# Kernel optimization log

Measured on AMD Instinct MI355X. Metric: run time of the kernel, lower is better.

## Reference

```python
import jax, jax.numpy as jnp
import numpy as np

B, N = 2, 2048
D_MODEL, HEADS = 512, 8
D_K = D_MODEL // HEADS
D_HIDDEN = 2048
MIN_SPREAD = 2.0
MIN_RBF = 1e-3
MAX_RBF = 1.0
LN_EPS = 1e-5


def setup_inputs() -> dict:
    key = jax.random.key(0)
    ks = jax.random.split(key, 12)
    xs = (6.0 / (D_K + D_MODEL)) ** 0.5
    q = jax.random.normal(ks[0], (B, N, D_MODEL), dtype=jnp.float32)
    k = jax.random.normal(ks[1], (B, N, D_MODEL), dtype=jnp.float32)
    v = jax.random.normal(ks[2], (B, N, D_MODEL), dtype=jnp.float32)
    coords = jax.random.normal(ks[3], (B, N, 3), dtype=jnp.float32) * 10.0
    mask = jnp.ones((B, N), dtype=bool)
    q_proj = jax.random.uniform(ks[4], (HEADS, D_MODEL, D_K), minval=-xs, maxval=xs)
    k_proj = jax.random.uniform(ks[5], (HEADS, D_MODEL, D_K), minval=-xs, maxval=xs)
    v_proj = jax.random.uniform(ks[6], (HEADS, D_MODEL, D_K), minval=-xs, maxval=xs)
    q_bias = jnp.zeros((HEADS, D_K))
    k_bias = jnp.zeros((HEADS, D_K))
    v_bias = jnp.zeros((HEADS, D_K))
    ow = (1.0 / D_MODEL) ** 0.5
    out_w = jax.random.uniform(ks[7], (D_MODEL, D_MODEL), minval=-ow, maxval=ow)
    spread_w = jnp.zeros((HEADS,))
    beta_w = jnp.zeros((HEADS,))
    ln1_g = jnp.ones((D_MODEL,)); ln1_b = jnp.zeros((D_MODEL,))
    ln2_g = jnp.ones((D_MODEL,)); ln2_b = jnp.zeros((D_MODEL,))
    w1 = jax.random.normal(ks[8], (D_MODEL, D_HIDDEN)) * 0.02
    b1 = jnp.zeros((D_HIDDEN,))
    w2 = jax.random.normal(ks[9], (D_HIDDEN, D_MODEL)) * 0.02
    b2 = jnp.zeros((D_MODEL,))
    return dict(q=q, k=k, v=v, coords=coords, mask=mask,
                q_proj=q_proj, k_proj=k_proj, v_proj=v_proj,
                q_bias=q_bias, k_bias=k_bias, v_bias=v_bias,
                out_w=out_w, spread_w=spread_w, beta_w=beta_w,
                ln1_g=ln1_g, ln1_b=ln1_b, ln2_g=ln2_g, ln2_b=ln2_b,
                w1=w1, b1=b1, w2=w2, b2=b2)


def _layernorm(x, g, b):
    mu = jnp.mean(x, axis=-1, keepdims=True)
    var = jnp.mean((x - mu) ** 2, axis=-1, keepdims=True)
    return (x - mu) * jax.lax.rsqrt(var + LN_EPS) * g + b


def _geo_attention(q, k, v, coords, mask,
                   q_proj, k_proj, v_proj, q_bias, k_bias, v_bias,
                   out_w, spread_w, beta_w):
    # per-head projections: [B,H,N,dk]
    Q = jnp.einsum('bnd,hdk->bhnk', q, q_proj) + q_bias[None, :, None, :]
    K = jnp.einsum('bnd,hdk->bhnk', k, k_proj) + k_bias[None, :, None, :]
    V = jnp.einsum('bnd,hdk->bhnk', v, v_proj) + v_bias[None, :, None, :]

    spreads = MIN_SPREAD + jnp.exp(spread_w)   # [H]
    betas = jnp.exp(beta_w)                    # [H]

    # pairwise squared distances [B,N,N]
    d2 = jnp.sum((coords[:, :, None, :] - coords[:, None, :, :]) ** 2, axis=-1)
    # per-head Gaussian RBF [B,H,N,N]
    rbf = jnp.exp(-d2[:, None, :, :] / (2.0 * spreads[None, :, None, None] ** 2))

    scores = jnp.einsum('bhnk,bhmk->bhnm', Q, K) / jnp.sqrt(jnp.float32(D_K))
    scores = betas[None, :, None, None] * rbf * scores

    # sparsity: keys with rbf outside [min_rbf, max_rbf] or padded are masked out
    valid = (rbf >= MIN_RBF) & (rbf <= MAX_RBF) & mask[:, None, None, :]
    scores = jnp.where(valid, scores, -jnp.inf)
    attn = jax.nn.softmax(scores, axis=-1)     # diagonal always valid (rbf=1)

    out = jnp.einsum('bhnm,bhmk->bhnk', attn, V)         # [B,H,N,dk]
    # torch: out.permute(0,2,3,1).reshape(B,N,d_model) -> (b,n,dk,h) layout
    out = jnp.transpose(out, (0, 2, 3, 1)).reshape(out.shape[0], out.shape[2], D_MODEL)
    return out @ out_w.T


def reference(q, k, v, coords, mask,
              q_proj, k_proj, v_proj, q_bias, k_bias, v_bias,
              out_w, spread_w, beta_w,
              ln1_g, ln1_b, ln2_g, ln2_b, w1, b1, w2, b2):
    attn_out = _geo_attention(q, k, v, coords, mask,
                              q_proj, k_proj, v_proj, q_bias, k_bias, v_bias,
                              out_w, spread_w, beta_w)
    x = _layernorm(q + attn_out, ln1_g, ln1_b)
    ffn = jax.nn.relu(x @ w1 + b1) @ w2 + b2
    x = _layernorm(x + ffn, ln2_g, ln2_b)
    return x
```

## Files before the change

### kernel.cpp

```cpp
#include <hip/hip_runtime.h>
#include <math.h>

typedef __attribute__((ext_vector_type(8))) short bf16x8;
typedef __attribute__((ext_vector_type(4))) float f32x4;

#define MFMA16(a,b,c) __builtin_amdgcn_mfma_f32_16x16x32_bf16((a),(b),(c),0,0,0)
#define LOG2E 1.44269504f

__device__ __forceinline__ unsigned short f2bf(float f) {
    union { float f; unsigned u; } x; x.f = f;
    unsigned r = x.u + 0x7FFFu + ((x.u >> 16) & 1u);
    return (unsigned short)(r >> 16);
}

__device__ __forceinline__ unsigned cvt_pk_bf16(float lo, float hi) {
    unsigned r;
    asm("v_cvt_pk_bf16_f32 %0, %1, %2" : "=v"(r) : "v"(lo), "v"(hi));
    return r;
}

__device__ __forceinline__ float exp2_fast(float x) {
    float r; asm("v_exp_f32 %0, %1" : "=v"(r) : "v"(x)); return r;
}

__device__ __forceinline__ void gload16(const unsigned short* g, unsigned short* l) {
    __builtin_amdgcn_global_load_lds(
        (const __attribute__((address_space(1))) void*)(unsigned long long)g,
        (__attribute__((address_space(3))) void*)(unsigned int)(unsigned long long)l,
        16, 0, 0);
}

__global__ __launch_bounds__(256) void cvt_qkv(
    const float* __restrict__ q, const float* __restrict__ k,
    const float* __restrict__ v,
    unsigned short* __restrict__ qb, unsigned short* __restrict__ kb,
    unsigned short* __restrict__ vb, int n)
{
    for (int i = blockIdx.x * 256 + threadIdx.x; i < n; i += gridDim.x * 256) {
        qb[i] = f2bf(q[i]); kb[i] = f2bf(k[i]); vb[i] = f2bf(v[i]);
    }
}

__global__ __launch_bounds__(256) void cvt_weights(
    const float* __restrict__ qp, const float* __restrict__ kp,
    const float* __restrict__ vp, const float* __restrict__ ow,
    const float* __restrict__ w1, const float* __restrict__ w2,
    const float* __restrict__ qbias, const float* __restrict__ kbias,
    const float* __restrict__ vbias,
    unsigned short* __restrict__ qpT, unsigned short* __restrict__ kpT,
    unsigned short* __restrict__ vpT, unsigned short* __restrict__ owT,
    unsigned short* __restrict__ w1T, unsigned short* __restrict__ w2T,
    float* __restrict__ biasC)
{
    const int NP = 262144;
    const int total = 4 * NP + 1048576 + 1048576 + 1536;
    for (int i = blockIdx.x * 256 + threadIdx.x; i < total; i += gridDim.x * 256) {
        if (i < 3 * NP) {
            int which = i / NP, r = i - which * NP;
            int n = r >> 9, d = r & 511;
            int h = n >> 6, kk = n & 63;
            const float* src = (which == 0) ? qp : (which == 1) ? kp : vp;
            unsigned short* dst = (which == 0) ? qpT : (which == 1) ? kpT : vpT;
            dst[r] = f2bf(src[(h << 15) + (d << 6) + kk]);
        } else if (i < 4 * NP) {
            int r = i - 3 * NP;
            int oi = r >> 9, f = r & 511;
            int h = f >> 6, kk = f & 63;
            owT[r] = f2bf(ow[(oi << 9) + (kk << 3) + h]);
        } else if (i < 4 * NP + 1048576) {
            int r = i - 4 * NP;
            int n = r >> 9, d = r & 511;
            w1T[r] = f2bf(w1[(d << 11) + n]);
        } else if (i < 4 * NP + 2097152) {
            int r = i - 4 * NP - 1048576;
            int n = r >> 11, d = r & 2047;
            w2T[r] = f2bf(w2[(d << 9) + n]);
        } else {
            int j = i - 4 * NP - 2097152;
            biasC[j] = (j < 512) ? qbias[j] : (j < 1024) ? kbias[j - 512] : vbias[j - 1024];
        }
    }
}

template<int BNT, int RELU, int SF32, int SB16, int SVTR, int SQKV>
__global__ __launch_bounds__(256) void gemm_bt(
    const unsigned short* __restrict__ Aq,
    const unsigned short* __restrict__ Ak,
    const unsigned short* __restrict__ Av,
    const unsigned short* __restrict__ Bt,
    const float* __restrict__ bias,
    float* __restrict__ Cf, unsigned short* __restrict__ Cb,
    unsigned short* __restrict__ Cb2, unsigned short* __restrict__ Cb3,
    int M, int N, int K)
{
    constexpr int BC = BNT / 32;
    __shared__ __align__(16) unsigned short As[128][64];
    __shared__ __align__(16) unsigned short Bs[BNT][64];
    const int tid = threadIdx.x;
    const int m0 = blockIdx.y << 7, n0 = blockIdx.x * BNT;
    const int wv = tid >> 6, lane = tid & 63;
    const int lrow = lane & 15, kg = lane >> 4;
    const int wr = (wv >> 1) << 6, wc = (wv & 1) * (BNT / 2);
    const int gr = lane >> 3, gc = (lane & 7) << 3;

    const unsigned short* A = Aq;
    if (SQKV) A = (n0 < 512) ? Aq : (n0 < 1024) ? Ak : Av;

    f32x4 acc[4][BC];
    const f32x4 z4 = {0.f, 0.f, 0.f, 0.f};
#pragma unroll
    for (int i = 0; i < 4; ++i)
#pragma unroll
        for (int j = 0; j < BC; ++j) acc[i][j] = z4;

    const int nkt = K >> 6;
    for (int kt = 0; kt < nkt; ++kt) {
        __syncthreads();
        const int k0 = kt << 6;
#pragma unroll
        for (int i = 0; i < 4; ++i) {
            const int r = (wv << 5) + (i << 3);
            gload16(&A[(long)(m0 + r + gr) * K + k0 + gc], &As[r][0]);
        }
#pragma unroll
        for (int i = 0; i < BNT / 32; ++i) {
            const int r = wv * (BNT / 4) + (i << 3);
            gload16(&Bt[(long)(n0 + r + gr) * K + k0 + gc], &Bs[r][0]);
        }
        __syncthreads();
#pragma unroll
        for (int ks = 0; ks < 2; ++ks) {
            const int koff = (ks << 5) + (kg << 3);
            bf16x8 af[4], bfr[BC];
#pragma unroll
            for (int mi = 0; mi < 4; ++mi)
                af[mi] = *(const bf16x8*)(&As[wr + (mi << 4) + lrow][koff]);
#pragma unroll
            for (int ni = 0; ni < BC; ++ni)
                bfr[ni] = *(const bf16x8*)(&Bs[wc + (ni << 4) + lrow][koff]);
#pragma unroll
            for (int mi = 0; mi < 4; ++mi)
#pragma unroll
                for (int ni = 0; ni < BC; ++ni)
                    acc[mi][ni] = MFMA16(af[mi], bfr[ni], acc[mi][ni]);
        }
    }

#pragma unroll
    for (int mi = 0; mi < 4; ++mi) {
#pragma unroll
        for (int ni = 0; ni < BC; ++ni) {
            const int col = n0 + wc + (ni << 4) + lrow;
            const float bv = bias ? bias[col] : 0.0f;
#pragma unroll
            for (int j = 0; j < 4; ++j) {
                const int row = m0 + wr + (mi << 4) + (kg << 2) + j;
                float val = acc[mi][ni][j] + bv;
                if (RELU) val = fmaxf(val, 0.0f);
                if (SF32) Cf[(long)row * N + col] = val;
                if (SB16) Cb[(long)row * N + col] = f2bf(val);
                if (SVTR)
                    Cb[((long)(row >> 11) << 20) + ((long)col << 11) + (row & 2047)] = f2bf(val);
                if (SQKV) {
                    if (n0 < 512)
                        Cb[(long)row * 512 + col] = f2bf(val);
                    else if (n0 < 1024)
                        Cb2[(long)row * 512 + (col - 512)] = f2bf(val);
                    else {
                        const int c2 = col - 1024;
                        Cb3[((long)(row >> 11) << 20) + ((long)c2 << 11) + (row & 2047)] = f2bf(val);
                    }
                }
            }
        }
    }
}

__global__ __launch_bounds__(256) void geo_attn(
    const unsigned short* __restrict__ Qh,
    const unsigned short* __restrict__ Kh,
    const unsigned short* __restrict__ VhT,
    const float* __restrict__ coords,
    const float* __restrict__ spread_w, const float* __restrict__ beta_w,
    unsigned short* __restrict__ Ob)
{
    __shared__ unsigned short Qs[64][72];
    __shared__ unsigned short Ks[64][72];
    __shared__ unsigned short Vs[64][72];
    __shared__ unsigned short Ps[4][16][72];
    __shared__ float4 ck4[64];

    const int tid = threadIdx.x;
    const int bid = blockIdx.x;
    const int swz = ((bid & 7) << 6) + (bid >> 3);
    const int bh = swz >> 5, qt = swz & 31;
    const int b = bh >> 3, h = bh & 7;
    const int wv = tid >> 6, lane = tid & 63;
    const int lq = lane & 15, kg = lane >> 4;
    const float NEG_INF = -__builtin_inff();
    const float THRL = 8.0f * LOG2E;
    const float RCUT = -9.96578428f;

    const float spread = 2.0f + __expf(spread_w[h]);
    const float inv2s2l = LOG2E / (2.0f * spread * spread);
    const float coefL = __expf(beta_w[h]) * 0.125f * LOG2E;

    {
        const long qbase = ((long)(b * 2048 + qt * 64)) * 512 + h * 64;
#pragma unroll
        for (int i = 0; i < 2; ++i) {
            int slot = tid + (i << 8);
            int r = slot >> 3, c = (slot & 7) << 3;
            *(int4*)(&Qs[r][c]) = *(const int4*)(&Qh[qbase + (long)r * 512 + c]);
        }
    }

    float cqx, cqy, cqz;
    {
        long ca = ((long)(b * 2048 + qt * 64 + wv * 16 + lq)) * 3;
        cqx = coords[ca]; cqy = coords[ca + 1]; cqz = coords[ca + 2];
    }

    float mrun = NEG_INF, lrun = 0.0f;
    f32x4 Oa[4];
    const f32x4 z4 = {0.f, 0.f, 0.f, 0.f};
#pragma unroll
    for (int nd = 0; nd < 4; ++nd) Oa[nd] = z4;

    const long kbase0 = ((long)b * 2048) * 512 + h * 64;
    const long vbase = ((long)(b * 8 + h)) * 131072;

    for (int kt = 0; kt < 32; ++kt) {
        __syncthreads();
        const int k0 = kt << 6;
#pragma unroll
        for (int i = 0; i < 2; ++i) {
            int slot = tid + (i << 8);
            int r = slot >> 3, c = (slot & 7) << 3;
            *(int4*)(&Ks[r][c]) = *(const int4*)(&Kh[kbase0 + (long)(k0 + r) * 512 + c]);
            *(int4*)(&Vs[r][c]) = *(const int4*)(&VhT[vbase + (long)r * 2048 + k0 + c]);
        }
        if (tid < 64) {
            long ca = ((long)(b * 2048 + k0 + tid)) * 3;
            ck4[tid] = make_float4(coords[ca], coords[ca + 1], coords[ca + 2], 0.0f);
        }
        __syncthreads();

        f32x4 t4[4];
#pragma unroll
        for (int ra = 0; ra < 4; ++ra) t4[ra] = z4;
#pragma unroll
        for (int ks = 0; ks < 2; ++ks) {
            const int koff = (ks << 5) + (kg << 3);
            bf16x8 bq = *(const bf16x8*)(&Qs[(wv << 4) + lq][koff]);
#pragma unroll
            for (int ra = 0; ra < 4; ++ra) {
                bf16x8 ak = *(const bf16x8*)(&Ks[(ra << 4) + lq][koff]);
                t4[ra] = MFMA16(ak, bq, t4[ra]);
            }
        }

        float tmax = NEG_INF;
#pragma unroll
        for (int ra = 0; ra < 4; ++ra) {
#pragma unroll
            for (int j = 0; j < 4; ++j) {
                float4 ck = ck4[(ra << 4) + (kg << 2) + j];
                float dx = cqx - ck.x, dy = cqy - ck.y, dz = cqz - ck.z;
                float d2 = dx * dx + dy * dy + dz * dz;
                float rexp = -d2 * inv2s2l;
                float rbf = exp2_fast(rexp);
                float val = (rexp >= RCUT) ? coefL * rbf * t4[ra][j] : NEG_INF;
                t4[ra][j] = val;
                tmax = fmaxf(tmax, val);
            }
        }
        tmax = fmaxf(tmax, __shfl_xor(tmax, 16, 64));
        tmax = fmaxf(tmax, __shfl_xor(tmax, 32, 64));

        const bool grow_any = __any(tmax > mrun + THRL);
        float psum = 0.0f;
        if (grow_any) {
            const float mn = fmaxf(mrun, tmax);
            const bool dead = (mn == NEG_INF);
            const float meff = dead ? 0.0f : mn;
            const float fcorr = dead ? 1.0f : exp2_fast(mrun - mn);
#pragma unroll
            for (int ra = 0; ra < 4; ++ra) {
#pragma unroll
                for (int j = 0; j < 4; ++j) {
                    float p = exp2_fast(t4[ra][j] - meff);
                    t4[ra][j] = p;
                    psum += p;
                }
            }
            psum += __shfl_xor(psum, 16, 64);
            psum += __shfl_xor(psum, 32, 64);
            mrun = mn;
            lrun = lrun * fcorr + psum;
            float fb[4];
#pragma unroll
            for (int j = 0; j < 4; ++j)
                fb[j] = __shfl(fcorr, (lane & 48) | ((kg << 2) + j), 64);
#pragma unroll
            for (int nd = 0; nd < 4; ++nd)
#pragma unroll
                for (int j = 0; j < 4; ++j)
                    Oa[nd][j] *= fb[j];
        } else {
            const float meff = (mrun == NEG_INF) ? 0.0f : mrun;
#pragma unroll
            for (int ra = 0; ra < 4; ++ra) {
#pragma unroll
                for (int j = 0; j < 4; ++j) {
                    float p = exp2_fast(t4[ra][j] - meff);
                    t4[ra][j] = p;
                    psum += p;
                }
            }
            psum += __shfl_xor(psum, 16, 64);
            psum += __shfl_xor(psum, 32, 64);
            lrun += psum;
        }

#pragma unroll
        for (int ra = 0; ra < 4; ++ra) {
            uint2 pk;
            pk.x = cvt_pk_bf16(t4[ra][0], t4[ra][1]);
            pk.y = cvt_pk_bf16(t4[ra][2], t4[ra][3]);
            *(uint2*)(&Ps[wv][lq][(ra << 4) + (kg << 2)]) = pk;
        }

#pragma unroll
        for (int ks = 0; ks < 2; ++ks) {
            const int koff = (ks << 5) + (kg << 3);
            bf16x8 ap = *(const bf16x8*)(&Ps[wv][lq][koff]);
#pragma unroll
            for (int nd = 0; nd < 4; ++nd) {
                bf16x8 bv = *(const bf16x8*)(&Vs[(nd << 4) + lq][koff]);
                Oa[nd] = MFMA16(ap, bv, Oa[nd]);
            }
        }
    }

    const float inv = 1.0f / lrun;
    float il[4];
#pragma unroll
    for (int j = 0; j < 4; ++j)
        il[j] = __shfl(inv, (lane & 48) | ((kg << 2) + j), 64);
    const long obase = ((long)(b * 2048 + qt * 64 + (wv << 4))) * 512 + h * 64;
#pragma unroll
    for (int nd = 0; nd < 4; ++nd)
#pragma unroll
        for (int j = 0; j < 4; ++j)
            Ob[obase + (long)((kg << 2) + j) * 512 + (nd << 4) + lq] =
                f2bf(Oa[nd][j] * il[j]);
}

template<int SB16>
__global__ __launch_bounds__(256) void ln_res(
    const float* __restrict__ X, const float* __restrict__ R,
    const float* __restrict__ g, const float* __restrict__ bb,
    float* __restrict__ Yf, unsigned short* __restrict__ Yb)
{
    const int wv = threadIdx.x >> 6, lane = threadIdx.x & 63;
    const long row = (long)blockIdx.x * 4 + wv;
    const float* xp = X + row * 512;
    const float* rp = R + row * 512;
    const int c0 = lane * 8;
    float4 a0 = *(const float4*)(xp + c0);
    float4 a1 = *(const float4*)(xp + c0 + 4);
    float4 r0 = *(const float4*)(rp + c0);
    float4 r1 = *(const float4*)(rp + c0 + 4);
    float v[8] = {a0.x + r0.x, a0.y + r0.y, a0.z + r0.z, a0.w + r0.w,
                  a1.x + r1.x, a1.y + r1.y, a1.z + r1.z, a1.w + r1.w};
    float s = 0.f, ss = 0.f;
#pragma unroll
    for (int i = 0; i < 8; ++i) { s += v[i]; ss += v[i] * v[i]; }
#pragma unroll
    for (int off = 1; off < 64; off <<= 1) {
        s += __shfl_xor(s, off, 64);
        ss += __shfl_xor(ss, off, 64);
    }
    const float mu = s * (1.0f / 512.0f);
    const float var = ss * (1.0f / 512.0f) - mu * mu;
    const float rstd = rsqrtf(var + 1e-5f);
#pragma unroll
    for (int i = 0; i < 8; ++i) {
        const int c = c0 + i;
        const float y = (v[i] - mu) * rstd * g[c] + bb[c];
        Yf[row * 512 + c] = y;
        if (SB16) Yb[row * 512 + c] = f2bf(y);
    }
}

extern "C" void kernel_launch(void* const* d_in, const int* in_sizes, int n_in,
                              void* d_out, int out_size, void* d_ws, size_t ws_size,
                              hipStream_t stream)
{
    const float* q      = (const float*)d_in[0];
    const float* k      = (const float*)d_in[1];
    const float* v      = (const float*)d_in[2];
    const float* coords = (const float*)d_in[3];
    const float* q_proj = (const float*)d_in[5];
    const float* k_proj = (const float*)d_in[6];
    const float* v_proj = (const float*)d_in[7];
    const float* q_bias = (const float*)d_in[8];
    const float* k_bias = (const float*)d_in[9];
    const float* v_bias = (const float*)d_in[10];
    const float* out_w  = (const float*)d_in[11];
    const float* spread_w = (const float*)d_in[12];
    const float* beta_w = (const float*)d_in[13];
    const float* ln1_g  = (const float*)d_in[14];
    const float* ln1_b  = (const float*)d_in[15];
    const float* ln2_g  = (const float*)d_in[16];
    const float* ln2_b  = (const float*)d_in[17];
    const float* w1     = (const float*)d_in[18];
    const float* b1     = (const float*)d_in[19];
    const float* w2     = (const float*)d_in[20];
    const float* b2     = (const float*)d_in[21];
    float* out = (float*)d_out;

    char* ws = (char*)d_ws;
    size_t off = 0;
    auto alloc = [&](size_t bytes) -> void* {
        void* p = ws + off;
        off += (bytes + 255) & ~(size_t)255;
        return p;
    };
    unsigned short* qb   = (unsigned short*)alloc(4096UL * 512 * 2);
    unsigned short* kb   = (unsigned short*)alloc(4096UL * 512 * 2);
    unsigned short* vb   = (unsigned short*)alloc(4096UL * 512 * 2);
    unsigned short* qpT  = (unsigned short*)alloc(512UL * 512 * 2);
    unsigned short* kpT  = (unsigned short*)alloc(512UL * 512 * 2);
    unsigned short* vpT  = (unsigned short*)alloc(512UL * 512 * 2);
    unsigned short* owT  = (unsigned short*)alloc(512UL * 512 * 2);
    unsigned short* w1T  = (unsigned short*)alloc(2048UL * 512 * 2);
    unsigned short* w2T  = (unsigned short*)alloc(512UL * 2048 * 2);
    float* biasC = (float*)alloc(1536UL * 4);
    unsigned short* Qp   = (unsigned short*)alloc(4096UL * 512 * 2);
    unsigned short* Kp   = (unsigned short*)alloc(4096UL * 512 * 2);
    unsigned short* VpT  = (unsigned short*)alloc(4096UL * 512 * 2);
    unsigned short* attnb= (unsigned short*)alloc(4096UL * 512 * 2);
    float* proj = (float*)alloc(4096UL * 512 * 4);
    float* x1   = (float*)alloc(4096UL * 512 * 4);
    unsigned short* x1b = (unsigned short*)alloc(4096UL * 512 * 2);
    unsigned short* hid = (unsigned short*)alloc(4096UL * 2048 * 2);
    float* ffn  = (float*)alloc(4096UL * 512 * 4);
    (void)ws_size; (void)in_sizes; (void)n_in; (void)out_size;

    cvt_qkv<<<2048, 256, 0, stream>>>(q, k, v, qb, kb, vb, 2097152);
    cvt_weights<<<2048, 256, 0, stream>>>(q_proj, k_proj, v_proj, out_w, w1, w2,
                                          q_bias, k_bias, v_bias,
                                          qpT, kpT, vpT, owT, w1T, w2T, biasC);

    gemm_bt<128, 0, 0, 0, 0, 1><<<dim3(12, 32), 256, 0, stream>>>(
        qb, kb, vb, qpT, biasC, nullptr, Qp, Kp, VpT, 4096, 1536, 512);

    geo_attn<<<512, 256, 0, stream>>>(Qp, Kp, VpT, coords, spread_w, beta_w, attnb);

    gemm_bt<64, 0, 1, 0, 0, 0><<<dim3(8, 32), 256, 0, stream>>>(
        attnb, nullptr, nullptr, owT, nullptr, proj, nullptr, nullptr, nullptr, 4096, 512, 512);
    ln_res<1><<<1024, 256, 0, stream>>>(proj, q, ln1_g, ln1_b, x1, x1b);

    gemm_bt<128, 1, 0, 1, 0, 0><<<dim3(16, 32), 256, 0, stream>>>(
        x1b, nullptr, nullptr, w1T, b1, nullptr, hid, nullptr, nullptr, 4096, 2048, 512);
    gemm_bt<64, 0, 1, 0, 0, 0><<<dim3(8, 32), 256, 0, stream>>>(
        hid, nullptr, nullptr, w2T, b2, ffn, nullptr, nullptr, nullptr, 4096, 512, 2048);
    ln_res<0><<<1024, 256, 0, stream>>>(ffn, x1, ln2_g, ln2_b, out, nullptr);
}
```

Measured before the change: 211.0 us.

## Fuse fp32 input conversion into QKV GEMM and tile-transpose FFN weights

```diff
diff --git a/kernel.cpp b/kernel.cpp
--- a/kernel.cpp
+++ b/kernel.cpp
@@ -23,37 +23,32 @@
     float r; asm("v_exp_f32 %0, %1" : "=v"(r) : "v"(x)); return r;
 }
 
-__device__ __forceinline__ void gload16(const unsigned short* g, unsigned short* l) {
-    __builtin_amdgcn_global_load_lds(
-        (const __attribute__((address_space(1))) void*)(unsigned long long)g,
-        (__attribute__((address_space(3))) void*)(unsigned int)(unsigned long long)l,
-        16, 0, 0);
-}
-
-__global__ __launch_bounds__(256) void cvt_qkv(
-    const float* __restrict__ q, const float* __restrict__ k,
-    const float* __restrict__ v,
-    unsigned short* __restrict__ qb, unsigned short* __restrict__ kb,
-    unsigned short* __restrict__ vb, int n)
-{
-    for (int i = blockIdx.x * 256 + threadIdx.x; i < n; i += gridDim.x * 256) {
-        qb[i] = f2bf(q[i]); kb[i] = f2bf(k[i]); vb[i] = f2bf(v[i]);
-    }
+__global__ __launch_bounds__(256) void transpose_w(
+    const float* __restrict__ in, unsigned short* __restrict__ outb, int R, int C)
+{
+    __shared__ float t[32][33];
+    const int tx = threadIdx.x & 31, ty = threadIdx.x >> 5;
+    const int c0 = blockIdx.x << 5, r0 = blockIdx.y << 5;
+#pragma unroll
+    for (int i = 0; i < 4; ++i)
+        t[ty + i * 8][tx] = in[(long)(r0 + ty + i * 8) * C + c0 + tx];
+    __syncthreads();
+#pragma unroll
+    for (int i = 0; i < 4; ++i)
+        outb[(long)(c0 + ty + i * 8) * R + r0 + tx] = f2bf(t[tx][ty + i * 8]);
 }
 
 __global__ __launch_bounds__(256) void cvt_weights(
     const float* __restrict__ qp, const float* __restrict__ kp,
     const float* __restrict__ vp, const float* __restrict__ ow,
-    const float* __restrict__ w1, const float* __restrict__ w2,
     const float* __restrict__ qbias, const float* __restrict__ kbias,
     const float* __restrict__ vbias,
     unsigned short* __restrict__ qpT, unsigned short* __restrict__ kpT,
     unsigned short* __restrict__ vpT, unsigned short* __restrict__ owT,
-    unsigned short* __restrict__ w1T, unsigned short* __restrict__ w2T,
     float* __restrict__ biasC)
 {
     const int NP = 262144;
-    const int total = 4 * NP + 1048576 + 1048576 + 1536;
+    const int total = 4 * NP + 1536;
     for (int i = blockIdx.x * 256 + threadIdx.x; i < total; i += gridDim.x * 256) {
         if (i < 3 * NP) {
             int which = i / NP, r = i - which * NP;
@@ -67,26 +62,18 @@
             int oi = r >> 9, f = r & 511;
             int h = f >> 6, kk = f & 63;
             owT[r] = f2bf(ow[(oi << 9) + (kk << 3) + h]);
-        } else if (i < 4 * NP + 1048576) {
-            int r = i - 4 * NP;
-            int n = r >> 9, d = r & 511;
-            w1T[r] = f2bf(w1[(d << 11) + n]);
-        } else if (i < 4 * NP + 2097152) {
-            int r = i - 4 * NP - 1048576;
-            int n = r >> 11, d = r & 2047;
-            w2T[r] = f2bf(w2[(d << 9) + n]);
         } else {
-            int j = i - 4 * NP - 2097152;
+            int j = i - 4 * NP;
             biasC[j] = (j < 512) ? qbias[j] : (j < 1024) ? kbias[j - 512] : vbias[j - 1024];
         }
     }
 }
 
-template<int BNT, int RELU, int SF32, int SB16, int SVTR, int SQKV>
+template<int BNT, int AF32, int RELU, int SF32, int SB16, int SVTR, int SQKV>
 __global__ __launch_bounds__(256) void gemm_bt(
-    const unsigned short* __restrict__ Aq,
-    const unsigned short* __restrict__ Ak,
-    const unsigned short* __restrict__ Av,
+    const void* __restrict__ Aq,
+    const void* __restrict__ Ak,
+    const void* __restrict__ Av,
     const unsigned short* __restrict__ Bt,
     const float* __restrict__ bias,
     float* __restrict__ Cf, unsigned short* __restrict__ Cb,
@@ -94,16 +81,15 @@
     int M, int N, int K)
 {
     constexpr int BC = BNT / 32;
-    __shared__ __align__(16) unsigned short As[128][64];
-    __shared__ __align__(16) unsigned short Bs[BNT][64];
+    __shared__ unsigned short As[128][72];
+    __shared__ unsigned short Bs[BNT][72];
     const int tid = threadIdx.x;
     const int m0 = blockIdx.y << 7, n0 = blockIdx.x * BNT;
     const int wv = tid >> 6, lane = tid & 63;
     const int lrow = lane & 15, kg = lane >> 4;
     const int wr = (wv >> 1) << 6, wc = (wv & 1) * (BNT / 2);
-    const int gr = lane >> 3, gc = (lane & 7) << 3;
-
-    const unsigned short* A = Aq;
+
+    const void* A = Aq;
     if (SQKV) A = (n0 < 512) ? Aq : (n0 < 1024) ? Ak : Av;
 
     f32x4 acc[4][BC];
@@ -119,13 +105,28 @@
         const int k0 = kt << 6;
 #pragma unroll
         for (int i = 0; i < 4; ++i) {
-            const int r = (wv << 5) + (i << 3);
-            gload16(&A[(long)(m0 + r + gr) * K + k0 + gc], &As[r][0]);
-        }
-#pragma unroll
-        for (int i = 0; i < BNT / 32; ++i) {
-            const int r = wv * (BNT / 4) + (i << 3);
-            gload16(&Bt[(long)(n0 + r + gr) * K + k0 + gc], &Bs[r][0]);
+            int slot = tid + (i << 8);
+            int r = slot >> 3, c = (slot & 7) << 3;
+            if (AF32) {
+                const float* Af = (const float*)A;
+                float4 a0 = *(const float4*)(&Af[(long)(m0 + r) * K + k0 + c]);
+                float4 a1 = *(const float4*)(&Af[(long)(m0 + r) * K + k0 + c + 4]);
+                int4 w;
+                w.x = (int)cvt_pk_bf16(a0.x, a0.y);
+                w.y = (int)cvt_pk_bf16(a0.z, a0.w);
+                w.z = (int)cvt_pk_bf16(a1.x, a1.y);
+                w.w = (int)cvt_pk_bf16(a1.z, a1.w);
+                *(int4*)(&As[r][c]) = w;
+            } else {
+                const unsigned short* Ab = (const unsigned short*)A;
+                *(int4*)(&As[r][c]) = *(const int4*)(&Ab[(long)(m0 + r) * K + k0 + c]);
+            }
+        }
+#pragma unroll
+        for (int i = 0; i < BC; ++i) {
+            int slot = tid + (i << 8);
+            int r = slot >> 3, c = (slot & 7) << 3;
+            *(int4*)(&Bs[r][c]) = *(const int4*)(&Bt[(long)(n0 + r) * K + k0 + c]);
         }
         __syncthreads();
 #pragma unroll
@@ -286,14 +287,13 @@
             const float meff = dead ? 0.0f : mn;
             const float fcorr = dead ? 1.0f : exp2_fast(mrun - mn);
 #pragma unroll
-            for (int ra = 0; ra < 4; ++ra) {
+            for (int ra = 0; ra < 4; ++ra)
 #pragma unroll
                 for (int j = 0; j < 4; ++j) {
                     float p = exp2_fast(t4[ra][j] - meff);
                     t4[ra][j] = p;
                     psum += p;
                 }
-            }
             psum += __shfl_xor(psum, 16, 64);
             psum += __shfl_xor(psum, 32, 64);
             mrun = mn;
@@ -310,14 +310,13 @@
         } else {
             const float meff = (mrun == NEG_INF) ? 0.0f : mrun;
 #pragma unroll
-            for (int ra = 0; ra < 4; ++ra) {
+            for (int ra = 0; ra < 4; ++ra)
 #pragma unroll
                 for (int j = 0; j < 4; ++j) {
                     float p = exp2_fast(t4[ra][j] - meff);
                     t4[ra][j] = p;
                     psum += p;
                 }
-            }
             psum += __shfl_xor(psum, 16, 64);
             psum += __shfl_xor(psum, 32, 64);
             lrun += psum;
@@ -428,9 +427,6 @@
         off += (bytes + 255) & ~(size_t)255;
         return p;
     };
-    unsigned short* qb   = (unsigned short*)alloc(4096UL * 512 * 2);
-    unsigned short* kb   = (unsigned short*)alloc(4096UL * 512 * 2);
-    unsigned short* vb   = (unsigned short*)alloc(4096UL * 512 * 2);
     unsigned short* qpT  = (unsigned short*)alloc(512UL * 512 * 2);
     unsigned short* kpT  = (unsigned short*)alloc(512UL * 512 * 2);
     unsigned short* vpT  = (unsigned short*)alloc(512UL * 512 * 2);
@@ -449,23 +445,24 @@
     float* ffn  = (float*)alloc(4096UL * 512 * 4);
     (void)ws_size; (void)in_sizes; (void)n_in; (void)out_size;
 
-    cvt_qkv<<<2048, 256, 0, stream>>>(q, k, v, qb, kb, vb, 2097152);
-    cvt_weights<<<2048, 256, 0, stream>>>(q_proj, k_proj, v_proj, out_w, w1, w2,
+    cvt_weights<<<2048, 256, 0, stream>>>(q_proj, k_proj, v_proj, out_w,
                                           q_bias, k_bias, v_bias,
-                                          qpT, kpT, vpT, owT, w1T, w2T, biasC);
-
-    gemm_bt<128, 0, 0, 0, 0, 1><<<dim3(12, 32), 256, 0, stream>>>(
-        qb, kb, vb, qpT, biasC, nullptr, Qp, Kp, VpT, 4096, 1536, 512);
+                                          qpT, kpT, vpT, owT, biasC);
+    transpose_w<<<dim3(64, 16), 256, 0, stream>>>(w1, w1T, 512, 2048);
+    transpose_w<<<dim3(16, 64), 256, 0, stream>>>(w2, w2T, 2048, 512);
+
+    gemm_bt<128, 1, 0, 0, 0, 0, 1><<<dim3(12, 32), 256, 0, stream>>>(
+        q, k, v, qpT, biasC, nullptr, Qp, Kp, VpT, 4096, 1536, 512);
 
     geo_attn<<<512, 256, 0, stream>>>(Qp, Kp, VpT, coords, spread_w, beta_w, attnb);
 
-    gemm_bt<64, 0, 1, 0, 0, 0><<<dim3(8, 32), 256, 0, stream>>>(
+    gemm_bt<64, 0, 0, 1, 0, 0, 0><<<dim3(8, 32), 256, 0, stream>>>(
         attnb, nullptr, nullptr, owT, nullptr, proj, nullptr, nullptr, nullptr, 4096, 512, 512);
     ln_res<1><<<1024, 256, 0, stream>>>(proj, q, ln1_g, ln1_b, x1, x1b);
 
-    gemm_bt<128, 1, 0, 1, 0, 0><<<dim3(16, 32), 256, 0, stream>>>(
+    gemm_bt<128, 0, 1, 0, 1, 0, 0><<<dim3(16, 32), 256, 0, stream>>>(
         x1b, nullptr, nullptr, w1T, b1, nullptr, hid, nullptr, nullptr, 4096, 2048, 512);
-    gemm_bt<64, 0, 1, 0, 0, 0><<<dim3(8, 32), 256, 0, stream>>>(
+    gemm_bt<64, 0, 0, 1, 0, 0, 0><<<dim3(8, 32), 256, 0, stream>>>(
         hid, nullptr, nullptr, w2T, b2, ffn, nullptr, nullptr, nullptr, 4096, 512, 2048);
     ln_res<0><<<1024, 256, 0, stream>>>(ffn, x1, ln2_g, ln2_b, out, nullptr);
 }
```

Result: faster. 196.6 us (-6.8%).
